# Performance work log

Measured on AMD Instinct MI355X. Metric: run time of the kernel, lower is better.

Reference implementation:

```python
import jax, jax.numpy as jnp
from jax import lax
import numpy as np

V, Dm, L, B = 32000, 1024, 1024, 4      # vocab, d_model, seq_len, batch
NL, E, H = 2, 8, 1024                    # layers, experts, expert_hidden
DS, DC, EXP = 16, 4, 2                   # d_state, d_conv, expand
DI = EXP * Dm                            # d_inner = 2048
DTR = Dm // 16                           # dt_rank = 64


def setup_inputs() -> dict:
    key = jax.random.key(0)
    ks = iter(jax.random.split(key, 48))
    def n(shape, s=0.02):
        return jax.random.normal(next(ks), shape, jnp.float32) * s
    inp = {
        "tokens": jax.random.randint(next(ks), (B, L), 1, V),
        "emb": jax.random.uniform(next(ks), (V, Dm), jnp.float32, -0.1, 0.1),
        "pos": n((1, L, Dm)),
        # per-layer stacked Mamba params
        "in_w": n((NL, 2 * DI, Dm)),
        "conv_w": n((NL, DI, 1, DC), 0.1),
        "conv_b": jnp.zeros((NL, DI)),
        "xp_w": n((NL, DTR + 2 * DS, DI)),
        "dt_w": n((NL, DI, DTR), 0.1),
        "dt_b": jnp.zeros((NL, DI)),
        "A_log": jnp.log(jnp.tile(jnp.arange(1, DS + 1, dtype=jnp.float32)[None, None, :], (NL, DI, 1))),
        "D_ssm": jnp.ones((NL, DI)),
        "out_w": n((NL, Dm, DI)),
        # layer norms
        "ln1_g": jnp.ones((NL, Dm)), "ln1_b": jnp.zeros((NL, Dm)),
        "ln2_g": jnp.ones((NL, Dm)), "ln2_b": jnp.zeros((NL, Dm)),
        # MoE
        "gate_w": n((NL, E, Dm)), "gate_b": jnp.zeros((NL, E)),
        "e_w1": n((NL, E, H, Dm)), "e_b1": jnp.zeros((NL, E, H)),
        "e_w2": n((NL, E, Dm, H)), "e_b2": jnp.zeros((NL, E, Dm)),
        # head
        "fc1_w": jax.random.uniform(next(ks), (128, Dm), jnp.float32, -0.1, 0.1),
        "fc1_b": jnp.zeros((128,)),
        "fc2_w": jax.random.uniform(next(ks), (2, 128), jnp.float32, -0.1, 0.1),
        "fc2_b": jnp.zeros((2,)),
    }
    return inp


def _ln(x, g, b, eps=1e-5):
    m = x.mean(-1, keepdims=True)
    v = ((x - m) ** 2).mean(-1, keepdims=True)
    return (x - m) * lax.rsqrt(v + eps) * g + b


def _mamba(x, in_w, conv_w, conv_b, xp_w, dt_w, dt_b, A_log, D_ssm, out_w):
    Bb = x.shape[0]
    u, z = jnp.split(x @ in_w.T, 2, axis=-1)  # [B,L,DI] each
    # causal depthwise conv over time
    uc = lax.conv_general_dilated(jnp.swapaxes(u, 1, 2), conv_w, (1,), [(DC - 1, 0)],
                                  feature_group_count=DI,
                                  dimension_numbers=("NCH", "OIH", "NCH")) + conv_b[None, :, None]
    u = jax.nn.silu(jnp.swapaxes(uc, 1, 2))  # [B,L,DI]
    dt, Bm, Cm = jnp.split(u @ xp_w.T, [DTR, DTR + DS], axis=-1)
    dt = jax.nn.softplus(dt @ dt_w.T + dt_b)  # [B,L,DI]
    A = -jnp.exp(A_log)  # [DI,DS]

    def step(h, inp):
        u_t, dt_t, B_t, C_t = inp  # [B,DI],[B,DI],[B,DS],[B,DS]
        h = jnp.exp(dt_t[..., None] * A) * h + (dt_t * u_t)[..., None] * B_t[:, None, :]
        return h, jnp.einsum("bdn,bn->bd", h, C_t)

    h0 = jnp.zeros((Bb, DI, DS), x.dtype)
    xs = tuple(jnp.swapaxes(a, 0, 1) for a in (u, dt, Bm, Cm))
    _, ys = lax.scan(step, h0, xs)
    y = jnp.swapaxes(ys, 0, 1) + u * D_ssm
    return (y * jax.nn.silu(z)) @ out_w.T


def _moe(x, gate_w, gate_b, w1, b1, w2, b2):
    Bb, Ll, Dd = x.shape
    xf = x.reshape(-1, Dd)
    gw = jax.nn.softmax(xf @ gate_w.T + gate_b, axis=-1)  # [N,E]
    top_w = jnp.max(gw, axis=-1)
    top_idx = jnp.argmax(gw, axis=-1)
    out = jnp.zeros_like(xf)
    for e in range(E):  # top-1 routing: only routed tokens keep expert e's output
        ye = jax.nn.relu(xf @ w1[e].T + b1[e]) @ w2[e].T + b2[e]
        out = out + jnp.where((top_idx == e)[:, None], top_w[:, None] * ye, 0.0)
    return out.reshape(Bb, Ll, Dd)


def reference(tokens, emb, pos, in_w, conv_w, conv_b, xp_w, dt_w, dt_b, A_log, D_ssm, out_w,
              ln1_g, ln1_b, ln2_g, ln2_b, gate_w, gate_b, e_w1, e_b1, e_w2, e_b2,
              fc1_w, fc1_b, fc2_w, fc2_b):
    x = emb[tokens] + pos[:, :tokens.shape[1], :]
    for l in range(NL):
        x = x + _ln(_mamba(x, in_w[l], conv_w[l], conv_b[l], xp_w[l], dt_w[l], dt_b[l],
                           A_log[l], D_ssm[l], out_w[l]), ln1_g[l], ln1_b[l])
        x = x + _ln(_moe(x, gate_w[l], gate_b[l], e_w1[l], e_b1[l], e_w2[l], e_b2[l]),
                    ln2_g[l], ln2_b[l])
    mask = (x.sum(-1) != 0)[..., None].astype(x.dtype)
    pooled = (x * mask).sum(1) / jnp.maximum(mask.sum(1), 1.0)
    h = jax.nn.relu(pooled @ fc1_w.T + fc1_b)
    return h @ fc2_w.T + fc2_b
```

## Files before the change

kernel.cpp:

```cpp
#include <hip/hip_runtime.h>
#include <hip/hip_bf16.h>

using bf = __hip_bfloat16;
typedef unsigned short u16;

#define V_   32000
#define DM   1024
#define LQ   1024
#define BB   4
#define NLAY 2
#define NE   8
#define HH   1024
#define DS   16
#define DC   4
#define DI   2048
#define DTR  64
#define NTOK (BB*LQ)

#define NC 16
#define CL (LQ/NC)

typedef __attribute__((ext_vector_type(8))) short s8v;
typedef __attribute__((ext_vector_type(4))) float f4v;

__device__ inline float tofl(float x) { return x; }
__device__ inline float tofl(bf x) { return __bfloat162float(x); }

template<typename T> __device__ inline T fromf(float v);
template<> __device__ inline float fromf<float>(float v) { return v; }
template<> __device__ inline bf fromf<bf>(float v) { return __float2bfloat16(v); }

__device__ inline u16 f2bfu(float x) {
    bf h = __float2bfloat16(x);
    return __builtin_bit_cast(u16, h);
}
__device__ inline float bfu2f(u16 u) {
    bf h = __builtin_bit_cast(bf, u);
    return __bfloat162float(h);
}

__device__ inline f4v mfma16(s8v a, s8v b, f4v c) {
    return __builtin_amdgcn_mfma_f32_16x16x32_bf16(a, b, c, 0, 0, 0);
}

__device__ __forceinline__ void gl2lds16(const u16* g, u16* l) {
    __builtin_amdgcn_global_load_lds(
        (const __attribute__((address_space(1))) unsigned int*)g,
        (__attribute__((address_space(3))) unsigned int*)l, 16, 0, 0);
}

__global__ __launch_bounds__(256) void split2_kernel(
    const float* __restrict__ in, int ldin,
    u16* __restrict__ out, int K)
{
    int id = blockIdx.x * 256 + threadIdx.x;
    int e4 = id * 4;
    int r = e4 / K;
    int k = e4 - r * K;
    float4 v = *(const float4*)(in + (size_t)r * ldin + k);
    int b = k >> 5, j = k & 31;
    ushort4 hi, lo;
    hi.x = f2bfu(v.x); lo.x = f2bfu(v.x - bfu2f(hi.x));
    hi.y = f2bfu(v.y); lo.y = f2bfu(v.y - bfu2f(hi.y));
    hi.z = f2bfu(v.z); lo.z = f2bfu(v.z - bfu2f(hi.z));
    hi.w = f2bfu(v.w); lo.w = f2bfu(v.w - bfu2f(hi.w));
    u16* o = out + (size_t)r * (2 * K) + b * 64 + j;
    *(ushort4*)o = hi;
    *(ushort4*)(o + 32) = lo;
}

__global__ __launch_bounds__(256) void zerof4_kernel(float4* __restrict__ p) {
    p[(size_t)blockIdx.x * 256 + threadIdx.x] = make_float4(0.f, 0.f, 0.f, 0.f);
}

__global__ __launch_bounds__(512) void gemm_pipe3(
    const u16* __restrict__ A, int lda,
    const u16* __restrict__ Bw, int ldb,
    bf* __restrict__ C, int ldc,
    int K32)
{
    __shared__ u16 LA[3][256 * 64];
    __shared__ u16 LB[3][128 * 64];

    int t = threadIdx.x, lane = t & 63, wv = t >> 6;
    int m0 = blockIdx.y * 256, n0 = blockIdx.x * 128;
    int wm = (wv >> 1) * 64, wn = (wv & 1) * 64;
    int fr = lane & 15, kq = lane >> 4;

    int lrow8 = lane >> 3;
    int lchunk = (lane & 7) ^ lrow8;
    const u16* Abase = A + (size_t)(m0 + wv * 32 + lrow8) * lda + lchunk * 8;
    const u16* Bbase = Bw + (size_t)(n0 + wv * 16 + lrow8) * ldb + lchunk * 8;

    f4v acc[4][4];
#pragma unroll
    for (int i = 0; i < 4; i++)
#pragma unroll
        for (int j = 0; j < 4; j++) acc[i][j] = 0.f;

    auto stage = [&](int q, int s) {
        const u16* ap = Abase + (size_t)q * 64;
#pragma unroll
        for (int j = 0; j < 4; j++)
            gl2lds16(ap + (size_t)(j * 8) * lda, &LA[s][(wv * 32 + j * 8) * 64]);
        const u16* bp = Bbase + (size_t)q * 64;
#pragma unroll
        for (int j = 0; j < 2; j++)
            gl2lds16(bp + (size_t)(j * 8) * ldb, &LB[s][(wv * 16 + j * 8) * 64]);
    };

    stage(0, 0);
    stage(1, 1);

    for (int q = 0; q < K32; ++q) {
        int s = q % 3;
        if (q + 1 < K32) asm volatile("s_waitcnt vmcnt(6)" ::: "memory");
        else             asm volatile("s_waitcnt vmcnt(0)" ::: "memory");
        __builtin_amdgcn_sched_barrier(0);
        __builtin_amdgcn_s_barrier();
        __builtin_amdgcn_sched_barrier(0);

        if (q + 2 < K32) stage(q + 2, (q + 2) % 3);

        s8v ah[4], al[4], bh[4], bl[4];
#pragma unroll
        for (int mi = 0; mi < 4; mi++) {
            int R = wm + mi * 16 + fr;
            int c = kq ^ (R & 7);
            ah[mi] = *(const s8v*)&LA[s][R * 64 + c * 8];
            al[mi] = *(const s8v*)&LA[s][R * 64 + (c ^ 4) * 8];
        }
#pragma unroll
        for (int ni = 0; ni < 4; ni++) {
            int R = wn + ni * 16 + fr;
            int c = kq ^ (R & 7);
            bh[ni] = *(const s8v*)&LB[s][R * 64 + c * 8];
            bl[ni] = *(const s8v*)&LB[s][R * 64 + (c ^ 4) * 8];
        }
        __builtin_amdgcn_s_setprio(1);
#pragma unroll
        for (int mi = 0; mi < 4; mi++)
#pragma unroll
            for (int ni = 0; ni < 4; ni++) {
                acc[mi][ni] = mfma16(ah[mi], bh[ni], acc[mi][ni]);
                acc[mi][ni] = mfma16(ah[mi], bl[ni], acc[mi][ni]);
                acc[mi][ni] = mfma16(al[mi], bh[ni], acc[mi][ni]);
            }
        __builtin_amdgcn_s_setprio(0);
        __builtin_amdgcn_sched_barrier(0);
    }

#pragma unroll
    for (int mi = 0; mi < 4; mi++) {
#pragma unroll
        for (int r4 = 0; r4 < 4; r4++) {
            int m = m0 + wm + mi * 16 + kq * 4 + r4;
#pragma unroll
            for (int ni = 0; ni < 4; ni++) {
                int n = n0 + wn + ni * 16 + fr;
                C[(size_t)m * ldc + n] = __float2bfloat16(acc[mi][ni][r4]);
            }
        }
    }
}

template<typename TC, int TERMS, int BN, int SPLITOUT = 0>
__global__ __launch_bounds__(256, 3) void gemm_s(
    const u16* __restrict__ A, int lda,
    const u16* __restrict__ Bw, int ldb,
    TC* __restrict__ C, int ldc,
    int M, int N, int K32,
    const float* __restrict__ bias, int epi,
    const int* __restrict__ cnt, const int* __restrict__ offs,
    const int* __restrict__ perm, int permmode,
    const float* __restrict__ scale,
    long long strideB_e, long long stride_bias_e,
    int nqz, int atomic_out)
{
    int zb = blockIdx.z;
    int Meff = M, rowoff = 0;
    int q0 = 0, q1 = K32;
    if (cnt) {
        Meff = cnt[zb];
        rowoff = offs[zb];
        Bw += (size_t)zb * strideB_e;
        if (bias) bias += (size_t)zb * stride_bias_e;
    } else if (nqz) {
        q0 = zb * nqz; q1 = q0 + nqz;
    }
    int m0 = blockIdx.y * 128;
    if (m0 >= Meff) return;
    int n0 = blockIdx.x * BN;

    constexpr int MI  = (BN == 128) ? 4 : 2;
    constexpr int NBR = BN / 64;

    __shared__ u16 AsH[128 * 32];
    __shared__ u16 AsL[(TERMS == 3) ? 128 * 32 : 8];
    __shared__ u16 BsH[BN * 32];
    __shared__ u16 BsL[BN * 32];

    int t = threadIdx.x, lane = t & 63, wv = t >> 6;
    int wm = (BN == 128) ? (wv & 1) * 64 : wv * 32;
    int wn = (BN == 128) ? (wv >> 1) * 64 : 0;
    int fr = lane & 15, kq = lane >> 4;
    int chunk = lane & 3;

    int arow[2], brow[2];
#pragma unroll
    for (int r = 0; r < 2; r++) {
        int m = m0 + r * 64 + wv * 16 + (lane >> 2);
        int ar = rowoff + ((m < Meff) ? m : 0);
        arow[r] = (permmode & 1) ? perm[ar] : ar;
    }
#pragma unroll
    for (int r = 0; r < NBR; r++) {
        int n = n0 + r * 64 + wv * 16 + (lane >> 2);
        brow[r] = (n < N) ? n : 0;
    }

    f4v acc[MI][4];
#pragma unroll
    for (int i = 0; i < MI; i++)
#pragma unroll
        for (int j = 0; j < 4; j++) acc[i][j] = 0.f;

    for (int q = q0; q < q1; ++q) {
        size_t acol = (TERMS == 3) ? ((size_t)q * 64 + chunk * 8)
                                   : ((size_t)q * 32 + chunk * 8);
        size_t bcol = (size_t)q * 64 + chunk * 8;
#pragma unroll
        for (int r = 0; r < 2; r++) {
            const u16* ap = A + (size_t)arow[r] * lda + acol;
            gl2lds16(ap, &AsH[(r * 64 + wv * 16) * 32]);
            if constexpr (TERMS == 3)
                gl2lds16(ap + 32, &AsL[(r * 64 + wv * 16) * 32]);
        }
#pragma unroll
        for (int r = 0; r < NBR; r++) {
            const u16* bp = Bw + (size_t)brow[r] * ldb + bcol;
            gl2lds16(bp, &BsH[(r * 64 + wv * 16) * 32]);
            gl2lds16(bp + 32, &BsL[(r * 64 + wv * 16) * 32]);
        }
        __syncthreads();

        s8v ahf[MI], bhf[4], blf[4];
#pragma unroll
        for (int mi = 0; mi < MI; mi++)
            ahf[mi] = *(const s8v*)&AsH[(wm + mi * 16 + fr) * 32 + kq * 8];
#pragma unroll
        for (int ni = 0; ni < 4; ni++)
            bhf[ni] = *(const s8v*)&BsH[(wn + ni * 16 + fr) * 32 + kq * 8];
#pragma unroll
        for (int ni = 0; ni < 4; ni++)
            blf[ni] = *(const s8v*)&BsL[(wn + ni * 16 + fr) * 32 + kq * 8];
#pragma unroll
        for (int mi = 0; mi < MI; mi++)
#pragma unroll
            for (int ni = 0; ni < 4; ni++) {
                acc[mi][ni] = mfma16(ahf[mi], bhf[ni], acc[mi][ni]);
                acc[mi][ni] = mfma16(ahf[mi], blf[ni], acc[mi][ni]);
            }
        if constexpr (TERMS == 3) {
            s8v alf[MI];
#pragma unroll
            for (int mi = 0; mi < MI; mi++)
                alf[mi] = *(const s8v*)&AsL[(wm + mi * 16 + fr) * 32 + kq * 8];
#pragma unroll
            for (int mi = 0; mi < MI; mi++)
#pragma unroll
                for (int ni = 0; ni < 4; ni++)
                    acc[mi][ni] = mfma16(alf[mi], bhf[ni], acc[mi][ni]);
        }
        __syncthreads();
    }

#pragma unroll
    for (int mi = 0; mi < MI; mi++) {
#pragma unroll
        for (int r4 = 0; r4 < 4; r4++) {
            int m = m0 + wm + mi * 16 + kq * 4 + r4;
            if (m >= Meff) continue;
            long long crow;
            float sc = 1.f;
            int ar = rowoff + m;
            if (permmode & 2) { int tok = perm[ar]; crow = tok; sc = scale[tok]; }
            else crow = ar;
#pragma unroll
            for (int ni = 0; ni < 4; ni++) {
                int n = n0 + wn + ni * 16 + fr;
                if (n >= N) continue;
                float v = acc[mi][ni][r4];
                if (bias) v += bias[n];
                if (epi == 1) v = (v > 20.f) ? v : log1pf(__expf(v));
                else if (epi == 2) v = fmaxf(v, 0.f);
                v *= sc;
                if constexpr (SPLITOUT) {
                    u16 hi = f2bfu(v);
                    u16 lo = f2bfu(v - bfu2f(hi));
                    size_t o = (size_t)crow * ldc + ((n >> 5) << 6) + (n & 31);
                    ((u16*)C)[o] = hi;
                    ((u16*)C)[o + 32] = lo;
                } else {
                    long long idx = crow * ldc + n;
                    if constexpr (sizeof(TC) == 4) {
                        if (atomic_out) atomicAdd((float*)C + idx, v);
                        else C[idx] = fromf<TC>(v);
                    } else {
                        C[idx] = fromf<TC>(v);
                    }
                }
            }
        }
    }
}

__global__ __launch_bounds__(256) void embed_kernel(
    const int* __restrict__ tokens, const float* __restrict__ emb,
    const float* __restrict__ pos, float* __restrict__ X)
{
    int id = blockIdx.x * 256 + threadIdx.x;
    int r = id >> 10, d = id & 1023;
    int l = r & (LQ - 1);
    int tok = tokens[r];
    X[id] = emb[(size_t)tok * DM + d] + pos[l * DM + d];
}

__global__ __launch_bounds__(256) void conv_kernel(
    const bf* __restrict__ XZ, const float* __restrict__ cw,
    const float* __restrict__ cb, bf* __restrict__ UC)
{
    int id = blockIdx.x * 256 + threadIdx.x;
    int d = id & (DI - 1);
    int r = id >> 11;
    int l = r & (LQ - 1);
    float acc = cb[d];
#pragma unroll
    for (int j = 0; j < DC; j++) {
        int ll = l - (DC - 1) + j;
        if (ll >= 0)
            acc += tofl(XZ[(size_t)(r - (DC - 1) + j) * (2 * DI) + d]) * cw[d * DC + j];
    }
    float sg = 1.f / (1.f + __expf(-acc));
    UC[id] = __float2bfloat16(acc * sg);
}

template<int PHASE>
__global__ __launch_bounds__(256) void scan_chunk(
    const bf* __restrict__ UC, float* __restrict__ DT,
    const float* __restrict__ W96, const bf* __restrict__ XZ,
    const float* __restrict__ A_log, const float* __restrict__ D_ssm,
    float* __restrict__ Hout, float* __restrict__ Stot,
    const float* __restrict__ Hin)
{
    int d = blockIdx.x * 256 + threadIdx.x;
    int c = blockIdx.y, b = blockIdx.z;
    float A[DS];
#pragma unroll
    for (int n = 0; n < DS; n++) A[n] = -__expf(A_log[d * DS + n]);
    float Dv = D_ssm[d];
    float h[DS];
    size_t hbase = ((size_t)(b * DI + d) * NC + c) * DS;
    if (PHASE == 0) {
#pragma unroll
        for (int n = 0; n < DS; n++) h[n] = 0.f;
    } else {
#pragma unroll
        for (int n = 0; n < DS; n += 4)
            *(float4*)&h[n] = *(const float4*)&Hin[hbase + n];
    }
    float S = 0.f;

    size_t rowb = (size_t)((b << 10) + c * CL);
    float u_c = tofl(UC[rowb * DI + d]);
    float dt_c = DT[rowb * DI + d];

    for (int t = 0; t < CL; t++) {
        size_t r = rowb + t;
        float u_n = 0.f, dt_n = 0.f;
        if (t + 1 < CL) {
            u_n = tofl(UC[(r + 1) * DI + d]);
            dt_n = DT[(r + 1) * DI + d];
        }
        float du = dt_c * u_c;
        if (PHASE == 0) S += dt_c;
        float y = 0.f;
#pragma unroll
        for (int n = 0; n < DS; n++) {
            float Bv = W96[r * 96 + DTR + n];
            h[n] = __expf(dt_c * A[n]) * h[n] + du * Bv;
            if (PHASE == 1) y += h[n] * W96[r * 96 + DTR + DS + n];
        }
        if (PHASE == 1) {
            float z = tofl(XZ[r * (2 * DI) + DI + d]);
            float sil = z / (1.f + __expf(-z));
            DT[r * DI + d] = (y + u_c * Dv) * sil;
        }
        u_c = u_n; dt_c = dt_n;
    }
    if (PHASE == 0) {
#pragma unroll
        for (int n = 0; n < DS; n += 4)
            *(float4*)&Hout[hbase + n] = *(const float4*)&h[n];
        Stot[(size_t)(b * DI + d) * NC + c] = S;
    }
}

__global__ __launch_bounds__(256) void scan_combine(
    const float* __restrict__ Hout, const float* __restrict__ Stot,
    const float* __restrict__ A_log, float* __restrict__ Hin)
{
    int id = blockIdx.x * 256 + threadIdx.x;
    int n = id & (DS - 1);
    int d = (id >> 4) & (DI - 1);
    int b = id >> 15;
    float A = -__expf(A_log[d * DS + n]);
    float h = 0.f;
    size_t base = (size_t)(b * DI + d) * NC * DS + n;
    size_t sbase = (size_t)(b * DI + d) * NC;
    for (int c = 0; c < NC; c++) {
        Hin[base + (size_t)c * DS] = h;
        h = __expf(A * Stot[sbase + c]) * h + Hout[base + (size_t)c * DS];
    }
}

__global__ __launch_bounds__(256) void ln_residual_kernel(
    float* __restrict__ X, const float* __restrict__ src,
    const float* __restrict__ g, const float* __restrict__ b,
    u16* __restrict__ xs, int* __restrict__ cntz)
{
    int row = blockIdx.x, tid = threadIdx.x;
    __shared__ float red[256];
    float v[4];
    float s = 0.f;
#pragma unroll
    for (int i = 0; i < 4; i++) { v[i] = src[(size_t)row * DM + tid + 256 * i]; s += v[i]; }
    red[tid] = s; __syncthreads();
    for (int o = 128; o > 0; o >>= 1) { if (tid < o) red[tid] += red[tid + o]; __syncthreads(); }
    float mean = red[0] * (1.f / DM);
    __syncthreads();
    float vs = 0.f;
#pragma unroll
    for (int i = 0; i < 4; i++) { float dd = v[i] - mean; vs += dd * dd; }
    red[tid] = vs; __syncthreads();
    for (int o = 128; o > 0; o >>= 1) { if (tid < o) red[tid] += red[tid + o]; __syncthreads(); }
    float rstd = rsqrtf(red[0] * (1.f / DM) + 1e-5f);
#pragma unroll
    for (int i = 0; i < 4; i++) {
        int c = tid + 256 * i;
        float nx = X[(size_t)row * DM + c] + (v[i] - mean) * rstd * g[c] + b[c];
        X[(size_t)row * DM + c] = nx;
        if (xs) {
            u16 hi = f2bfu(nx);
            u16 lo = f2bfu(nx - bfu2f(hi));
            size_t o2 = (size_t)row * (2 * DM) + ((c >> 5) << 6) + (c & 31);
            xs[o2] = hi;
            xs[o2 + 32] = lo;
        }
    }
    if (cntz && row == 0 && tid < 8) cntz[tid] = 0;
}

__global__ __launch_bounds__(64) void gate_kernel(
    const float* __restrict__ X, const float* __restrict__ gw, const float* __restrict__ gb,
    int* __restrict__ top_idx, float* __restrict__ top_w, int* __restrict__ cnt)
{
    int n = blockIdx.x;
    int lane = threadIdx.x;
    float acc[NE] = {};
    for (int k = lane; k < DM; k += 64) {
        float xv = X[(size_t)n * DM + k];
#pragma unroll
        for (int e = 0; e < NE; e++) acc[e] += xv * gw[e * DM + k];
    }
#pragma unroll
    for (int e = 0; e < NE; e++)
        for (int o = 32; o > 0; o >>= 1) acc[e] += __shfl_down(acc[e], o);
    if (lane == 0) {
        float logits[NE];
        float best = -1e30f; int bi = 0;
#pragma unroll
        for (int e = 0; e < NE; e++) {
            logits[e] = acc[e] + gb[e];
            if (logits[e] > best) { best = logits[e]; bi = e; }
        }
        float s = 0.f;
#pragma unroll
        for (int e = 0; e < NE; e++) s += __expf(logits[e] - best);
        top_idx[n] = bi;
        top_w[n] = 1.f / s;
        atomicAdd(&cnt[bi], 1);
    }
}

__global__ void offsets_kernel(const int* __restrict__ cnt, int* __restrict__ offs, int* __restrict__ pos)
{
    if (threadIdx.x == 0) {
        int a = 0;
        for (int e = 0; e < NE; e++) { offs[e] = a; a += cnt[e]; pos[e] = 0; }
        offs[NE] = a;
    }
}

__global__ __launch_bounds__(256) void scatter_kernel(
    const int* __restrict__ top_idx, const int* __restrict__ offs,
    int* __restrict__ pos, int* __restrict__ perm)
{
    int n = blockIdx.x * 256 + threadIdx.x;
    if (n >= NTOK) return;
    int e = top_idx[n];
    int slot = atomicAdd(&pos[e], 1);
    perm[offs[e] + slot] = n;
}

__global__ __launch_bounds__(256) void rowmask_kernel(const float* __restrict__ X, float* __restrict__ maskf)
{
    int row = blockIdx.x, tid = threadIdx.x;
    __shared__ float red[256];
    float s = 0.f;
    for (int i = tid; i < DM; i += 256) s += X[(size_t)row * DM + i];
    red[tid] = s; __syncthreads();
    for (int o = 128; o > 0; o >>= 1) { if (tid < o) red[tid] += red[tid + o]; __syncthreads(); }
    if (tid == 0) maskf[row] = (red[0] != 0.f) ? 1.f : 0.f;
}

__global__ __launch_bounds__(256) void cntb_kernel(const float* __restrict__ maskf, float* __restrict__ cntb)
{
    int b = blockIdx.x, tid = threadIdx.x;
    __shared__ float red[256];
    float s = 0.f;
    for (int i = tid; i < LQ; i += 256) s += maskf[b * LQ + i];
    red[tid] = s; __syncthreads();
    for (int o = 128; o > 0; o >>= 1) { if (tid < o) red[tid] += red[tid + o]; __syncthreads(); }
    if (tid == 0) cntb[b] = red[0];
}

__global__ __launch_bounds__(256) void pooled_kernel(
    const float* __restrict__ X, const float* __restrict__ maskf,
    const float* __restrict__ cntb, float* __restrict__ pooled)
{
    int d = blockIdx.x * 256 + threadIdx.x;
    int b = blockIdx.y;
    float s = 0.f;
    for (int l = 0; l < LQ; l++)
        s += X[(size_t)((b << 10) + l) * DM + d] * maskf[(b << 10) + l];
    pooled[b * DM + d] = s / fmaxf(cntb[b], 1.f);
}

__global__ __launch_bounds__(128) void head_kernel(
    const float* __restrict__ pooled,
    const float* __restrict__ fc1w, const float* __restrict__ fc1b,
    const float* __restrict__ fc2w, const float* __restrict__ fc2b,
    float* __restrict__ out)
{
    int b = blockIdx.x;
    int j = threadIdx.x;
    __shared__ float hbuf[128];
    float acc = fc1b[j];
    for (int k = 0; k < DM; k++) acc += pooled[b * DM + k] * fc1w[j * DM + k];
    hbuf[j] = fmaxf(acc, 0.f);
    __syncthreads();
    if (j < 2) {
        float o = fc2b[j];
        for (int k = 0; k < 128; k++) o += hbuf[k] * fc2w[j * 128 + k];
        out[b * 2 + j] = o;
    }
}

extern "C" void kernel_launch(void* const* d_in, const int* in_sizes, int n_in,
                              void* d_out, int out_size, void* d_ws, size_t ws_size,
                              hipStream_t stream)
{
    const int*   tokens = (const int*)d_in[0];
    const float* emb    = (const float*)d_in[1];
    const float* pos    = (const float*)d_in[2];
    const float* in_w   = (const float*)d_in[3];
    const float* conv_w = (const float*)d_in[4];
    const float* conv_b = (const float*)d_in[5];
    const float* xp_w   = (const float*)d_in[6];
    const float* dt_w   = (const float*)d_in[7];
    const float* dt_b   = (const float*)d_in[8];
    const float* A_log  = (const float*)d_in[9];
    const float* D_ssm  = (const float*)d_in[10];
    const float* out_w  = (const float*)d_in[11];
    const float* ln1_g  = (const float*)d_in[12];
    const float* ln1_b  = (const float*)d_in[13];
    const float* ln2_g  = (const float*)d_in[14];
    const float* ln2_b  = (const float*)d_in[15];
    const float* gate_w = (const float*)d_in[16];
    const float* gate_b = (const float*)d_in[17];
    const float* e_w1   = (const float*)d_in[18];
    const float* e_b1   = (const float*)d_in[19];
    const float* e_w2   = (const float*)d_in[20];
    const float* e_b2   = (const float*)d_in[21];
    const float* fc1_w  = (const float*)d_in[22];
    const float* fc1_b  = (const float*)d_in[23];
    const float* fc2_w  = (const float*)d_in[24];
    const float* fc2_b  = (const float*)d_in[25];
    float* outp = (float*)d_out;

    char* wsb = (char*)d_ws;
    size_t off = 0;
    auto alloc = [&](size_t bytes) { char* p = wsb + off; off += (bytes + 255) & ~(size_t)255; return p; };
    float* X    = (float*)alloc((size_t)NTOK * DM * 4);
    char* xzraw = (char*)alloc((size_t)NTOK * 2 * DI * 2);
    char* ucraw = (char*)alloc((size_t)NTOK * DI * 2);
    float* W96  = (float*)alloc((size_t)NTOK * 96 * 4);
    char* dtraw = (char*)alloc((size_t)NTOK * DI * 4);
    float* Hout = (float*)alloc((size_t)BB * DI * NC * DS * 4);
    float* Hin  = (float*)alloc((size_t)BB * DI * NC * DS * 4);
    float* Stot = (float*)alloc((size_t)BB * DI * NC * 4);
    float* top_w  = (float*)alloc(NTOK * 4);
    float* maskf  = (float*)alloc(NTOK * 4);
    float* pooled = (float*)alloc(BB * DM * 4);
    float* cntb   = (float*)alloc(64);
    int* top_idx  = (int*)alloc(NTOK * 4);
    int* perm     = (int*)alloc(NTOK * 4);
    int* cnt      = (int*)alloc(64);
    int* offs     = (int*)alloc(64);
    int* posc     = (int*)alloc(64);

    bf*    XZ   = (bf*)xzraw;
    bf*    UC   = (bf*)ucraw;
    float* DT   = (float*)dtraw;
    u16*   XS   = (u16*)ucraw;
    u16*   DTS  = (u16*)xzraw;
    u16*   H1S  = (u16*)(xzraw + (size_t)NTOK * HH * 4);
    float* MAM1 = (float*)ucraw;
    float* MAM2 = (float*)xzraw;
    u16*   WB   = (u16*)dtraw;
    u16*   WDT  = (u16*)Hin;
    u16*   W96S = (u16*)Hout;

    embed_kernel<<<(NTOK * DM) / 256, 256, 0, stream>>>(tokens, emb, pos, X);

    for (int lay = 0; lay < NLAY; lay++) {
        const float* in_w_l   = in_w   + (size_t)lay * 2 * DI * DM;
        const float* conv_w_l = conv_w + (size_t)lay * DI * DC;
        const float* conv_b_l = conv_b + (size_t)lay * DI;
        const float* xp_w_l   = xp_w   + (size_t)lay * 96 * DI;
        const float* dt_w_l   = dt_w   + (size_t)lay * DI * DTR;
        const float* dt_b_l   = dt_b   + (size_t)lay * DI;
        const float* A_log_l  = A_log  + (size_t)lay * DI * DS;
        const float* D_ssm_l  = D_ssm  + (size_t)lay * DI;
        const float* out_w_l  = out_w  + (size_t)lay * DM * DI;
        const float* gate_w_l = gate_w + (size_t)lay * NE * DM;
        const float* gate_b_l = gate_b + (size_t)lay * NE;
        const float* e_w1_l   = e_w1   + (size_t)lay * NE * HH * DM;
        const float* e_b1_l   = e_b1   + (size_t)lay * NE * HH;
        const float* e_w2_l   = e_w2   + (size_t)lay * NE * DM * HH;
        const float* e_b2_l   = e_b2   + (size_t)lay * NE * DM;

        if (lay == 0)
            split2_kernel<<<(NTOK * DM) / 1024, 256, 0, stream>>>(X, DM, XS, DM);
        split2_kernel<<<(2 * DI * DM) / 1024, 256, 0, stream>>>(in_w_l, DM, WB, DM);
        gemm_pipe3<<<dim3(2 * DI / 128, NTOK / 256, 1), 512, 0, stream>>>(
            XS, 2 * DM, WB, 2 * DM, XZ, 2 * DI, DM / 32);

        conv_kernel<<<(NTOK * DI) / 256, 256, 0, stream>>>(XZ, conv_w_l, conv_b_l, UC);

        zerof4_kernel<<<(NTOK * 96) / 1024, 256, 0, stream>>>((float4*)W96);
        split2_kernel<<<(96 * DI) / 1024, 256, 0, stream>>>(xp_w_l, DI, WB, DI);
        gemm_s<float, 2, 128><<<dim3(1, 32, 8), 256, 0, stream>>>(
            (const u16*)UC, DI, WB, 2 * DI, W96, 96, NTOK, 96, DI / 32,
            nullptr, 0, nullptr, nullptr, nullptr, 0, nullptr, 0, 0, (DI / 32) / 8, 1);

        split2_kernel<<<(DI * DTR) / 1024, 256, 0, stream>>>(dt_w_l, DTR, WDT, DTR);
        split2_kernel<<<(NTOK * DTR) / 1024, 256, 0, stream>>>(W96, 96, W96S, DTR);
        gemm_s<float, 3, 128><<<dim3(16, 32, 1), 256, 0, stream>>>(
            W96S, 2 * DTR, WDT, 2 * DTR, DT, DI, NTOK, DI, DTR / 32,
            dt_b_l, 1, nullptr, nullptr, nullptr, 0, nullptr, 0, 0, 0, 0);

        scan_chunk<0><<<dim3(DI / 256, NC, BB), 256, 0, stream>>>(
            UC, DT, W96, XZ, A_log_l, D_ssm_l, Hout, Stot, nullptr);
        scan_combine<<<(BB * DI * DS) / 256, 256, 0, stream>>>(Hout, Stot, A_log_l, Hin);
        scan_chunk<1><<<dim3(DI / 256, NC, BB), 256, 0, stream>>>(
            UC, DT, W96, XZ, A_log_l, D_ssm_l, Hout, Stot, Hin);

        split2_kernel<<<(NTOK * DI) / 1024, 256, 0, stream>>>(DT, DI, DTS, DI);
        split2_kernel<<<(DM * DI) / 1024, 256, 0, stream>>>(out_w_l, DI, WB, DI);
        gemm_s<float, 3, 128><<<dim3(8, 32, 1), 256, 0, stream>>>(
            DTS, 2 * DI, WB, 2 * DI, MAM1, DM, NTOK, DM, DI / 32,
            nullptr, 0, nullptr, nullptr, nullptr, 0, nullptr, 0, 0, 0, 0);

        ln_residual_kernel<<<NTOK, 256, 0, stream>>>(
            X, MAM1, ln1_g + lay * DM, ln1_b + lay * DM, XS, cnt);

        gate_kernel<<<NTOK, 64, 0, stream>>>(X, gate_w_l, gate_b_l, top_idx, top_w, cnt);
        offsets_kernel<<<1, 1, 0, stream>>>(cnt, offs, posc);
        scatter_kernel<<<NTOK / 256, 256, 0, stream>>>(top_idx, offs, posc, perm);

        split2_kernel<<<((size_t)NE * HH * DM) / 1024, 256, 0, stream>>>(e_w1_l, DM, WB, DM);
        gemm_s<u16, 3, 128, 1><<<dim3(8, 32, NE), 256, 0, stream>>>(
            XS, 2 * DM, WB, 2 * DM, H1S, 2 * HH, NTOK, HH, DM / 32,
            e_b1_l, 2, cnt, offs, perm, 1, nullptr,
            (long long)HH * 2 * DM, (long long)HH, 0, 0);

        split2_kernel<<<((size_t)NE * DM * HH) / 1024, 256, 0, stream>>>(e_w2_l, HH, WB, HH);
        gemm_s<float, 3, 128><<<dim3(8, 32, NE), 256, 0, stream>>>(
            H1S, 2 * HH, WB, 2 * HH, MAM2, DM, NTOK, DM, HH / 32,
            e_b2_l, 0, cnt, offs, perm, 2, top_w,
            (long long)DM * 2 * HH, (long long)DM, 0, 0);

        ln_residual_kernel<<<NTOK, 256, 0, stream>>>(
            X, MAM2, ln2_g + lay * DM, ln2_b + lay * DM, XS, nullptr);
    }

    rowmask_kernel<<<NTOK, 256, 0, stream>>>(X, maskf);
    cntb_kernel<<<BB, 256, 0, stream>>>(maskf, cntb);
    pooled_kernel<<<dim3(DM / 256, BB, 1), 256, 0, stream>>>(X, maskf, cntb, pooled);
    head_kernel<<<BB, 128, 0, stream>>>(pooled, fc1_w, fc1_b, fc2_w, fc2_b, outp);
}
```

Measured before the change: 1.803 ms.

## Fuse split conversions, compact MoE block map, interleave GEMM staging, parallelize pooling

The embed and scan kernels now write the bf16 hi/lo split layouts directly, which drops separate split2 passes. The MoE GEMMs use a compact block map built in offsets_kernel instead of launching blocks for every expert, and gemm_pipe3 gains block swizzling plus global-to-LDS staging interleaved with per-column MFMA phases. The conv kernel is vectorized to two channels per thread, and pooling is split across 8 sequence chunks combined with atomics. The risks are more barriers inside the GEMM loop, a __syncthreads inside the scan loop, atomic nondeterminism in pooling, and buffer aliasing changes (DTS now lives in DT's storage, and WBX in XZ's).

```diff
diff --git a/kernel.cpp b/kernel.cpp
--- a/kernel.cpp
+++ b/kernel.cpp
@@ -83,7 +83,11 @@
     __shared__ u16 LB[3][128 * 64];
 
     int t = threadIdx.x, lane = t & 63, wv = t >> 6;
-    int m0 = blockIdx.y * 256, n0 = blockIdx.x * 128;
+    int lin = blockIdx.y * gridDim.x + blockIdx.x;
+    int cpx = (gridDim.x * gridDim.y) >> 3;
+    int lin2 = (lin & 7) * cpx + (lin >> 3);
+    int bx = lin2 % gridDim.x, by = lin2 / gridDim.x;
+    int m0 = by * 256, n0 = bx * 128;
     int wm = (wv >> 1) * 64, wn = (wv & 1) * 64;
     int fr = lane & 15, kq = lane >> 4;
 
@@ -98,56 +102,73 @@
 #pragma unroll
         for (int j = 0; j < 4; j++) acc[i][j] = 0.f;
 
-    auto stage = [&](int q, int s) {
+    auto stageA2 = [&](int q, int s, int half) {
         const u16* ap = Abase + (size_t)q * 64;
 #pragma unroll
-        for (int j = 0; j < 4; j++)
+        for (int j = half * 2; j < half * 2 + 2; j++)
             gl2lds16(ap + (size_t)(j * 8) * lda, &LA[s][(wv * 32 + j * 8) * 64]);
+    };
+    auto stageB2 = [&](int q, int s) {
         const u16* bp = Bbase + (size_t)q * 64;
 #pragma unroll
         for (int j = 0; j < 2; j++)
             gl2lds16(bp + (size_t)(j * 8) * ldb, &LB[s][(wv * 16 + j * 8) * 64]);
     };
 
-    stage(0, 0);
-    stage(1, 1);
+    stageA2(0, 0, 0); stageA2(0, 0, 1); stageB2(0, 0);
+    stageA2(1, 1, 0); stageA2(1, 1, 1); stageB2(1, 1);
+    asm volatile("s_waitcnt vmcnt(6)" ::: "memory");
+    __builtin_amdgcn_sched_barrier(0);
+    __builtin_amdgcn_s_barrier();
 
     for (int q = 0; q < K32; ++q) {
         int s = q % 3;
-        if (q + 1 < K32) asm volatile("s_waitcnt vmcnt(6)" ::: "memory");
-        else             asm volatile("s_waitcnt vmcnt(0)" ::: "memory");
-        __builtin_amdgcn_sched_barrier(0);
-        __builtin_amdgcn_s_barrier();
-        __builtin_amdgcn_sched_barrier(0);
-
-        if (q + 2 < K32) stage(q + 2, (q + 2) % 3);
-
-        s8v ah[4], al[4], bh[4], bl[4];
-#pragma unroll
-        for (int mi = 0; mi < 4; mi++) {
-            int R = wm + mi * 16 + fr;
-            int c = kq ^ (R & 7);
-            ah[mi] = *(const s8v*)&LA[s][R * 64 + c * 8];
-            al[mi] = *(const s8v*)&LA[s][R * 64 + (c ^ 4) * 8];
-        }
-#pragma unroll
-        for (int ni = 0; ni < 4; ni++) {
-            int R = wn + ni * 16 + fr;
-            int c = kq ^ (R & 7);
-            bh[ni] = *(const s8v*)&LB[s][R * 64 + c * 8];
-            bl[ni] = *(const s8v*)&LB[s][R * 64 + (c ^ 4) * 8];
-        }
-        __builtin_amdgcn_s_setprio(1);
-#pragma unroll
-        for (int mi = 0; mi < 4; mi++)
-#pragma unroll
-            for (int ni = 0; ni < 4; ni++) {
-                acc[mi][ni] = mfma16(ah[mi], bh[ni], acc[mi][ni]);
-                acc[mi][ni] = mfma16(ah[mi], bl[ni], acc[mi][ni]);
-                acc[mi][ni] = mfma16(al[mi], bh[ni], acc[mi][ni]);
+        int s2 = (q + 2) % 3;
+
+        s8v ah[4], al[4];
+#pragma unroll
+        for (int p = 0; p < 4; p++) {
+            if (p == 0) {
+#pragma unroll
+                for (int mi = 0; mi < 4; mi++) {
+                    int R = wm + mi * 16 + fr;
+                    int c = kq ^ (R & 7);
+                    ah[mi] = *(const s8v*)&LA[s][R * 64 + c * 8];
+                    al[mi] = *(const s8v*)&LA[s][R * 64 + (c ^ 4) * 8];
+                }
             }
-        __builtin_amdgcn_s_setprio(0);
-        __builtin_amdgcn_sched_barrier(0);
+            s8v bh, bl;
+            {
+                int R = wn + p * 16 + fr;
+                int c = kq ^ (R & 7);
+                bh = *(const s8v*)&LB[s][R * 64 + c * 8];
+                bl = *(const s8v*)&LB[s][R * 64 + (c ^ 4) * 8];
+            }
+            if (q + 2 < K32) {
+                if (p == 0) stageA2(q + 2, s2, 0);
+                else if (p == 1) stageA2(q + 2, s2, 1);
+                else if (p == 2) stageB2(q + 2, s2);
+            }
+            __builtin_amdgcn_s_barrier();
+            asm volatile("s_waitcnt lgkmcnt(0)" ::: "memory");
+            __builtin_amdgcn_sched_barrier(0);
+            __builtin_amdgcn_s_setprio(1);
+#pragma unroll
+            for (int mi = 0; mi < 4; mi++) {
+                acc[mi][p] = mfma16(ah[mi], bh, acc[mi][p]);
+                acc[mi][p] = mfma16(ah[mi], bl, acc[mi][p]);
+                acc[mi][p] = mfma16(al[mi], bh, acc[mi][p]);
+            }
+            __builtin_amdgcn_s_setprio(0);
+            __builtin_amdgcn_sched_barrier(0);
+            if (p < 3) __builtin_amdgcn_s_barrier();
+        }
+        if (q + 1 < K32) {
+            if (q + 2 < K32) asm volatile("s_waitcnt vmcnt(6)" ::: "memory");
+            else             asm volatile("s_waitcnt vmcnt(0)" ::: "memory");
+            __builtin_amdgcn_sched_barrier(0);
+            __builtin_amdgcn_s_barrier();
+        }
     }
 
 #pragma unroll
@@ -175,20 +196,28 @@
     const int* __restrict__ perm, int permmode,
     const float* __restrict__ scale,
     long long strideB_e, long long stride_bias_e,
-    int nqz, int atomic_out)
-{
-    int zb = blockIdx.z;
+    int nqz, int atomic_out,
+    const int* __restrict__ bmap)
+{
+    int e = blockIdx.z, m0;
+    if (bmap) {
+        int by = blockIdx.y;
+        if (by >= bmap[0]) return;
+        e = bmap[1 + 2 * by];
+        m0 = bmap[2 + 2 * by] * 128;
+    } else {
+        m0 = blockIdx.y * 128;
+    }
     int Meff = M, rowoff = 0;
     int q0 = 0, q1 = K32;
     if (cnt) {
-        Meff = cnt[zb];
-        rowoff = offs[zb];
-        Bw += (size_t)zb * strideB_e;
-        if (bias) bias += (size_t)zb * stride_bias_e;
+        Meff = cnt[e];
+        rowoff = offs[e];
+        Bw += (size_t)e * strideB_e;
+        if (bias) bias += (size_t)e * stride_bias_e;
     } else if (nqz) {
-        q0 = zb * nqz; q1 = q0 + nqz;
-    }
-    int m0 = blockIdx.y * 128;
+        q0 = e * nqz; q1 = q0 + nqz;
+    }
     if (m0 >= Meff) return;
     int n0 = blockIdx.x * BN;
 
@@ -317,13 +346,20 @@
 
 __global__ __launch_bounds__(256) void embed_kernel(
     const int* __restrict__ tokens, const float* __restrict__ emb,
-    const float* __restrict__ pos, float* __restrict__ X)
+    const float* __restrict__ pos, float* __restrict__ X,
+    u16* __restrict__ xs)
 {
     int id = blockIdx.x * 256 + threadIdx.x;
     int r = id >> 10, d = id & 1023;
     int l = r & (LQ - 1);
     int tok = tokens[r];
-    X[id] = emb[(size_t)tok * DM + d] + pos[l * DM + d];
+    float val = emb[(size_t)tok * DM + d] + pos[l * DM + d];
+    X[id] = val;
+    u16 hi = f2bfu(val);
+    u16 lo = f2bfu(val - bfu2f(hi));
+    size_t o2 = (size_t)r * (2 * DM) + ((d >> 5) << 6) + (d & 31);
+    xs[o2] = hi;
+    xs[o2 + 32] = lo;
 }
 
 __global__ __launch_bounds__(256) void conv_kernel(
@@ -331,18 +367,25 @@
     const float* __restrict__ cb, bf* __restrict__ UC)
 {
     int id = blockIdx.x * 256 + threadIdx.x;
-    int d = id & (DI - 1);
-    int r = id >> 11;
+    int d = (id & (DI / 2 - 1)) * 2;
+    int r = id >> 10;
     int l = r & (LQ - 1);
-    float acc = cb[d];
+    float a0 = cb[d], a1 = cb[d + 1];
 #pragma unroll
     for (int j = 0; j < DC; j++) {
         int ll = l - (DC - 1) + j;
-        if (ll >= 0)
-            acc += tofl(XZ[(size_t)(r - (DC - 1) + j) * (2 * DI) + d]) * cw[d * DC + j];
-    }
-    float sg = 1.f / (1.f + __expf(-acc));
-    UC[id] = __float2bfloat16(acc * sg);
+        if (ll >= 0) {
+            const u16* p = (const u16*)XZ + (size_t)(r - (DC - 1) + j) * (2 * DI) + d;
+            ushort2 uv = *(const ushort2*)p;
+            a0 += bfu2f(uv.x) * cw[d * DC + j];
+            a1 += bfu2f(uv.y) * cw[(d + 1) * DC + j];
+        }
+    }
+    float s0 = a0 / (1.f + __expf(-a0));
+    float s1 = a1 / (1.f + __expf(-a1));
+    ushort2 ov;
+    ov.x = f2bfu(s0); ov.y = f2bfu(s1);
+    *(ushort2*)((u16*)UC + (size_t)r * DI + d) = ov;
 }
 
 template<int PHASE>
@@ -351,8 +394,11 @@
     const float* __restrict__ W96, const bf* __restrict__ XZ,
     const float* __restrict__ A_log, const float* __restrict__ D_ssm,
     float* __restrict__ Hout, float* __restrict__ Stot,
-    const float* __restrict__ Hin)
-{
+    const float* __restrict__ Hin,
+    u16* __restrict__ DTS, int* __restrict__ cntz)
+{
+    if (PHASE == 0 && blockIdx.x == 0 && blockIdx.y == 0 && blockIdx.z == 0
+        && threadIdx.x < 8) cntz[threadIdx.x] = 0;
     int d = blockIdx.x * 256 + threadIdx.x;
     int c = blockIdx.y, b = blockIdx.z;
     float A[DS];
@@ -394,7 +440,13 @@
         if (PHASE == 1) {
             float z = tofl(XZ[r * (2 * DI) + DI + d]);
             float sil = z / (1.f + __expf(-z));
-            DT[r * DI + d] = (y + u_c * Dv) * sil;
+            float yv = (y + u_c * Dv) * sil;
+            __syncthreads();
+            u16 hi = f2bfu(yv);
+            u16 lo = f2bfu(yv - bfu2f(hi));
+            size_t o2 = r * (2 * DI) + ((d >> 5) << 6) + (d & 31);
+            DTS[o2] = hi;
+            DTS[o2 + 32] = lo;
         }
         u_c = u_n; dt_c = dt_n;
     }
@@ -427,7 +479,7 @@
 __global__ __launch_bounds__(256) void ln_residual_kernel(
     float* __restrict__ X, const float* __restrict__ src,
     const float* __restrict__ g, const float* __restrict__ b,
-    u16* __restrict__ xs, int* __restrict__ cntz)
+    u16* __restrict__ xs)
 {
     int row = blockIdx.x, tid = threadIdx.x;
     __shared__ float red[256];
@@ -450,15 +502,12 @@
         int c = tid + 256 * i;
         float nx = X[(size_t)row * DM + c] + (v[i] - mean) * rstd * g[c] + b[c];
         X[(size_t)row * DM + c] = nx;
-        if (xs) {
-            u16 hi = f2bfu(nx);
-            u16 lo = f2bfu(nx - bfu2f(hi));
-            size_t o2 = (size_t)row * (2 * DM) + ((c >> 5) << 6) + (c & 31);
-            xs[o2] = hi;
-            xs[o2 + 32] = lo;
-        }
-    }
-    if (cntz && row == 0 && tid < 8) cntz[tid] = 0;
+        u16 hi = f2bfu(nx);
+        u16 lo = f2bfu(nx - bfu2f(hi));
+        size_t o2 = (size_t)row * (2 * DM) + ((c >> 5) << 6) + (c & 31);
+        xs[o2] = hi;
+        xs[o2 + 32] = lo;
+    }
 }
 
 __global__ __launch_bounds__(64) void gate_kernel(
@@ -493,12 +542,19 @@
     }
 }
 
-__global__ void offsets_kernel(const int* __restrict__ cnt, int* __restrict__ offs, int* __restrict__ pos)
+__global__ void offsets_kernel(const int* __restrict__ cnt, int* __restrict__ offs,
+                               int* __restrict__ pos, int* __restrict__ bmap)
 {
     if (threadIdx.x == 0) {
         int a = 0;
         for (int e = 0; e < NE; e++) { offs[e] = a; a += cnt[e]; pos[e] = 0; }
         offs[NE] = a;
+        int nb = 0;
+        for (int e = 0; e < NE; e++)
+            for (int yb = 0; yb * 128 < cnt[e]; yb++) {
+                bmap[1 + 2 * nb] = e; bmap[2 + 2 * nb] = yb; nb++;
+            }
+        bmap[0] = nb;
     }
 }
 
@@ -524,7 +580,9 @@
     if (tid == 0) maskf[row] = (red[0] != 0.f) ? 1.f : 0.f;
 }
 
-__global__ __launch_bounds__(256) void cntb_kernel(const float* __restrict__ maskf, float* __restrict__ cntb)
+__global__ __launch_bounds__(256) void cntb_kernel(const float* __restrict__ maskf,
+                                                   float* __restrict__ cntb,
+                                                   float* __restrict__ pooled)
 {
     int b = blockIdx.x, tid = threadIdx.x;
     __shared__ float red[256];
@@ -533,6 +591,7 @@
     red[tid] = s; __syncthreads();
     for (int o = 128; o > 0; o >>= 1) { if (tid < o) red[tid] += red[tid + o]; __syncthreads(); }
     if (tid == 0) cntb[b] = red[0];
+    for (int i = tid; i < DM; i += 256) pooled[b * DM + i] = 0.f;
 }
 
 __global__ __launch_bounds__(256) void pooled_kernel(
@@ -541,10 +600,11 @@
 {
     int d = blockIdx.x * 256 + threadIdx.x;
     int b = blockIdx.y;
+    int l0 = blockIdx.z * (LQ / 8);
     float s = 0.f;
-    for (int l = 0; l < LQ; l++)
+    for (int l = l0; l < l0 + LQ / 8; l++)
         s += X[(size_t)((b << 10) + l) * DM + d] * maskf[(b << 10) + l];
-    pooled[b * DM + d] = s / fmaxf(cntb[b], 1.f);
+    atomicAdd(&pooled[b * DM + d], s / fmaxf(cntb[b], 1.f));
 }
 
 __global__ __launch_bounds__(128) void head_kernel(
@@ -619,12 +679,14 @@
     int* cnt      = (int*)alloc(64);
     int* offs     = (int*)alloc(64);
     int* posc     = (int*)alloc(64);
+    int* bmap     = (int*)alloc(512);
 
     bf*    XZ   = (bf*)xzraw;
     bf*    UC   = (bf*)ucraw;
     float* DT   = (float*)dtraw;
     u16*   XS   = (u16*)ucraw;
-    u16*   DTS  = (u16*)xzraw;
+    u16*   DTS  = (u16*)dtraw;
+    u16*   WBX  = (u16*)xzraw;
     u16*   H1S  = (u16*)(xzraw + (size_t)NTOK * HH * 4);
     float* MAM1 = (float*)ucraw;
     float* MAM2 = (float*)xzraw;
@@ -632,7 +694,7 @@
     u16*   WDT  = (u16*)Hin;
     u16*   W96S = (u16*)Hout;
 
-    embed_kernel<<<(NTOK * DM) / 256, 256, 0, stream>>>(tokens, emb, pos, X);
+    embed_kernel<<<(NTOK * DM) / 256, 256, 0, stream>>>(tokens, emb, pos, X, XS);
 
     for (int lay = 0; lay < NLAY; lay++) {
         const float* in_w_l   = in_w   + (size_t)lay * 2 * DI * DM;
@@ -651,63 +713,60 @@
         const float* e_w2_l   = e_w2   + (size_t)lay * NE * DM * HH;
         const float* e_b2_l   = e_b2   + (size_t)lay * NE * DM;
 
-        if (lay == 0)
-            split2_kernel<<<(NTOK * DM) / 1024, 256, 0, stream>>>(X, DM, XS, DM);
         split2_kernel<<<(2 * DI * DM) / 1024, 256, 0, stream>>>(in_w_l, DM, WB, DM);
         gemm_pipe3<<<dim3(2 * DI / 128, NTOK / 256, 1), 512, 0, stream>>>(
             XS, 2 * DM, WB, 2 * DM, XZ, 2 * DI, DM / 32);
 
-        conv_kernel<<<(NTOK * DI) / 256, 256, 0, stream>>>(XZ, conv_w_l, conv_b_l, UC);
+        conv_kernel<<<(NTOK * DI / 2) / 256, 256, 0, stream>>>(XZ, conv_w_l, conv_b_l, UC);
 
         zerof4_kernel<<<(NTOK * 96) / 1024, 256, 0, stream>>>((float4*)W96);
         split2_kernel<<<(96 * DI) / 1024, 256, 0, stream>>>(xp_w_l, DI, WB, DI);
         gemm_s<float, 2, 128><<<dim3(1, 32, 8), 256, 0, stream>>>(
             (const u16*)UC, DI, WB, 2 * DI, W96, 96, NTOK, 96, DI / 32,
-            nullptr, 0, nullptr, nullptr, nullptr, 0, nullptr, 0, 0, (DI / 32) / 8, 1);
+            nullptr, 0, nullptr, nullptr, nullptr, 0, nullptr, 0, 0, (DI / 32) / 8, 1, nullptr);
 
         split2_kernel<<<(DI * DTR) / 1024, 256, 0, stream>>>(dt_w_l, DTR, WDT, DTR);
         split2_kernel<<<(NTOK * DTR) / 1024, 256, 0, stream>>>(W96, 96, W96S, DTR);
         gemm_s<float, 3, 128><<<dim3(16, 32, 1), 256, 0, stream>>>(
             W96S, 2 * DTR, WDT, 2 * DTR, DT, DI, NTOK, DI, DTR / 32,
-            dt_b_l, 1, nullptr, nullptr, nullptr, 0, nullptr, 0, 0, 0, 0);
+            dt_b_l, 1, nullptr, nullptr, nullptr, 0, nullptr, 0, 0, 0, 0, nullptr);
 
         scan_chunk<0><<<dim3(DI / 256, NC, BB), 256, 0, stream>>>(
-            UC, DT, W96, XZ, A_log_l, D_ssm_l, Hout, Stot, nullptr);
+            UC, DT, W96, XZ, A_log_l, D_ssm_l, Hout, Stot, nullptr, nullptr, cnt);
         scan_combine<<<(BB * DI * DS) / 256, 256, 0, stream>>>(Hout, Stot, A_log_l, Hin);
         scan_chunk<1><<<dim3(DI / 256, NC, BB), 256, 0, stream>>>(
-            UC, DT, W96, XZ, A_log_l, D_ssm_l, Hout, Stot, Hin);
-
-        split2_kernel<<<(NTOK * DI) / 1024, 256, 0, stream>>>(DT, DI, DTS, DI);
-        split2_kernel<<<(DM * DI) / 1024, 256, 0, stream>>>(out_w_l, DI, WB, DI);
+            UC, DT, W96, XZ, A_log_l, D_ssm_l, Hout, Stot, Hin, DTS, nullptr);
+
+        split2_kernel<<<(DM * DI) / 1024, 256, 0, stream>>>(out_w_l, DI, WBX, DI);
         gemm_s<float, 3, 128><<<dim3(8, 32, 1), 256, 0, stream>>>(
-            DTS, 2 * DI, WB, 2 * DI, MAM1, DM, NTOK, DM, DI / 32,
-            nullptr, 0, nullptr, nullptr, nullptr, 0, nullptr, 0, 0, 0, 0);
+            DTS, 2 * DI, WBX, 2 * DI, MAM1, DM, NTOK, DM, DI / 32,
+            nullptr, 0, nullptr, nullptr, nullptr, 0, nullptr, 0, 0, 0, 0, nullptr);
 
         ln_residual_kernel<<<NTOK, 256, 0, stream>>>(
-            X, MAM1, ln1_g + lay * DM, ln1_b + lay * DM, XS, cnt);
+            X, MAM1, ln1_g + lay * DM, ln1_b + lay * DM, XS);
 
         gate_kernel<<<NTOK, 64, 0, stream>>>(X, gate_w_l, gate_b_l, top_idx, top_w, cnt);
-        offsets_kernel<<<1, 1, 0, stream>>>(cnt, offs, posc);
+        offsets_kernel<<<1, 1, 0, stream>>>(cnt, offs, posc, bmap);
         scatter_kernel<<<NTOK / 256, 256, 0, stream>>>(top_idx, offs, posc, perm);
 
         split2_kernel<<<((size_t)NE * HH * DM) / 1024, 256, 0, stream>>>(e_w1_l, DM, WB, DM);
-        gemm_s<u16, 3, 128, 1><<<dim3(8, 32, NE), 256, 0, stream>>>(
+        gemm_s<u16, 3, 128, 1><<<dim3(8, 40, 1), 256, 0, stream>>>(
             XS, 2 * DM, WB, 2 * DM, H1S, 2 * HH, NTOK, HH, DM / 32,
             e_b1_l, 2, cnt, offs, perm, 1, nullptr,
-            (long long)HH * 2 * DM, (long long)HH, 0, 0);
+            (long long)HH * 2 * DM, (long long)HH, 0, 0, bmap);
 
         split2_kernel<<<((size_t)NE * DM * HH) / 1024, 256, 0, stream>>>(e_w2_l, HH, WB, HH);
-        gemm_s<float, 3, 128><<<dim3(8, 32, NE), 256, 0, stream>>>(
+        gemm_s<float, 3, 128><<<dim3(8, 40, 1), 256, 0, stream>>>(
             H1S, 2 * HH, WB, 2 * HH, MAM2, DM, NTOK, DM, HH / 32,
             e_b2_l, 0, cnt, offs, perm, 2, top_w,
-            (long long)DM * 2 * HH, (long long)DM, 0, 0);
+            (long long)DM * 2 * HH, (long long)DM, 0, 0, bmap);
 
         ln_residual_kernel<<<NTOK, 256, 0, stream>>>(
-            X, MAM2, ln2_g + lay * DM, ln2_b + lay * DM, XS, nullptr);
+            X, MAM2, ln2_g + lay * DM, ln2_b + lay * DM, XS);
     }
 
     rowmask_kernel<<<NTOK, 256, 0, stream>>>(X, maskf);
-    cntb_kernel<<<BB, 256, 0, stream>>>(maskf, cntb);
-    pooled_kernel<<<dim3(DM / 256, BB, 1), 256, 0, stream>>>(X, maskf, cntb, pooled);
+    cntb_kernel<<<BB, 256, 0, stream>>>(maskf, cntb, pooled);
+    pooled_kernel<<<dim3(DM / 256, BB, 8), 256, 0, stream>>>(X, maskf, cntb, pooled);
     head_kernel<<<BB, 128, 0, stream>>>(pooled, fc1_w, fc1_b, fc2_w, fc2_b, outp);
 }
```

Result: no change. 1.781 ms (-1.2%).
